# Kernel tuning notes

Measured on AMD Instinct MI355X. Metric: run time of the kernel, lower is better.

Reference implementation:

```python
import jax, jax.numpy as jnp
import numpy as np
from functools import partial

IMAGE_SIZE = 256
ORIG_SIZE = 1024
NEAR, FAR = 0.1, 100.0
CHUNK = 100  # faces processed per scan step to bound memory


def setup_inputs():
    key = jax.random.key(0)
    kv, kf = jax.random.split(key)
    B, V, F = 4, 5000, 10000
    verts = jax.random.normal(kv, (B, V, 3), jnp.float32) * 0.4
    verts = verts.at[..., 2].add(2.5)  # object in front of camera (+z)
    faces = jax.random.randint(kf, (B, F, 3), 0, V)
    fx = fy = float(ORIG_SIZE)
    cx = cy = ORIG_SIZE / 2.0
    K = jnp.broadcast_to(jnp.array([[fx, 0., cx], [0., fy, cy], [0., 0., 1.]], jnp.float32), (B, 3, 3))
    R = jnp.broadcast_to(jnp.eye(3, dtype=jnp.float32), (B, 3, 3))
    t = jnp.zeros((B, 1, 3), jnp.float32)
    dist_coeffs = jnp.zeros((B, 5), jnp.float32)
    return {"vertices": verts, "faces": faces, "K": K, "R": R, "t": t, "dist_coeffs": dist_coeffs}


def projection(vertices, K, R, t, dist_coeffs, orig_size, eps=1e-9):
    # vertices: [B,V,3]; matmul(vertices, R^T) + t, OpenCV distortion, intrinsics, NDC
    v = jnp.einsum('bvj,bij->bvi', vertices, R) + t
    x, y, z = v[..., 0], v[..., 1], v[..., 2]
    x_ = x / (z + eps)
    y_ = y / (z + eps)
    k1, k2, p1, p2, k3 = [dist_coeffs[:, i:i + 1] for i in range(5)]
    r2 = x_ * x_ + y_ * y_
    rad = 1. + k1 * r2 + k2 * r2 * r2 + k3 * r2 * r2 * r2
    x__ = x_ * rad + 2. * p1 * x_ * y_ + p2 * (r2 + 2. * x_ * x_)
    y__ = y_ * rad + p1 * (r2 + 2. * y_ * y_) + 2. * p2 * x_ * y_
    vv = jnp.stack([x__, y__, jnp.ones_like(z)], axis=-1)
    vv = jnp.einsum('bvj,bij->bvi', vv, K)
    u, vc = vv[..., 0], vv[..., 1]
    vc = orig_size - vc  # image y points down
    u = 2. * (u - orig_size / 2.) / orig_size
    vc = 2. * (vc - orig_size / 2.) / orig_size
    return jnp.stack([u, vc, z], axis=-1)  # [B,V,3] in NDC xy, camera z


def vertices_to_faces(vertices, faces):
    # vertices [B,V,3], faces [B,F,3] -> [B,F,3,3]
    return jnp.take_along_axis(vertices[:, :, None, :], faces[:, :, :, None], axis=1)


def rasterize_depth(face_verts, image_size, near, far):
    # face_verts: [B,F,3,3]; z-buffer min of barycentric-interpolated 1/z depth
    B, F = face_verts.shape[:2]
    pad = (-F) % CHUNK
    fv = jnp.pad(face_verts, ((0, 0), (0, pad), (0, 0), (0, 0)))  # padded faces are degenerate
    n_chunks = (F + pad) // CHUNK
    fv = fv.reshape(B, n_chunks, CHUNK, 3, 3).transpose(1, 0, 2, 3, 4)  # [n,B,C,3,3]
    ps = (2. * jnp.arange(image_size, dtype=jnp.float32) + 1. - image_size) / image_size
    xp = ps[None, None, None, :]  # [1,1,1,W]
    yp = ps[None, None, :, None]  # [1,1,H,1]
    eps = 1e-8

    def step(zbuf, chunk):  # chunk [B,C,3,3]
        x = chunk[..., 0]
        y = chunk[..., 1]
        z = chunk[..., 2]
        x0, x1, x2 = (x[..., i, None, None] for i in range(3))
        y0, y1, y2 = (y[..., i, None, None] for i in range(3))
        z0, z1, z2 = (z[..., i, None, None] for i in range(3))
        denom = (y1 - y2) * (x0 - x2) + (x2 - x1) * (y0 - y2)
        ok = jnp.abs(denom) > eps
        safe_d = jnp.where(ok, denom, 1.)
        w0 = ((y1 - y2) * (xp - x2) + (x2 - x1) * (yp - y2)) / safe_d  # [B,C,H,W]
        w1 = ((y2 - y0) * (xp - x2) + (x0 - x2) * (yp - y2)) / safe_d
        w2 = 1. - w0 - w1
        inside = (w0 >= 0.) & (w1 >= 0.) & (w2 >= 0.) & ok
        zs0 = jnp.where(z0 > eps, z0, 1.)
        zs1 = jnp.where(z1 > eps, z1, 1.)
        zs2 = jnp.where(z2 > eps, z2, 1.)
        zinv = w0 / zs0 + w1 / zs1 + w2 / zs2
        zp = 1. / jnp.where(zinv > eps, zinv, 1.)
        valid = inside & (zp > near) & (zp < far) & (z0 > eps) & (z1 > eps) & (z2 > eps)
        zp = jnp.where(valid, zp, far)
        zbuf = jnp.minimum(zbuf, jnp.min(zp, axis=1))  # min over faces in chunk
        return zbuf, None

    zbuf0 = jnp.full((B, image_size, image_size), far, dtype=face_verts.dtype)
    zbuf, _ = jax.lax.scan(step, zbuf0, fv)
    return zbuf[:, ::-1, :]  # flip vertically to image convention


def reference(vertices, faces, K, R, t, dist_coeffs):
    # fill_back: append faces with reversed winding
    faces_fb = jnp.concatenate([faces, faces[:, :, ::-1]], axis=1)
    v_ndc = projection(vertices, K, R, t, dist_coeffs, float(ORIG_SIZE))
    fverts = vertices_to_faces(v_ndc, faces_fb)  # [B,2F,3,3]
    return rasterize_depth(fverts, IMAGE_SIZE, NEAR, FAR)  # [B,H,W] depth map
```

## Files before the change

### kernel.cpp

```cpp
#include <hip/hip_runtime.h>

#define IMG 256
#define TW 32
#define TH 32
#define TILES 64
#define SUBSPLIT 16
#define RSUB 8
#define BIGF 1e30f

typedef float v4f __attribute__((ext_vector_type(4)));

__device__ __forceinline__ float ndc(int i) { return (2.0f*i + 1.0f - IMG) * (1.0f/IMG); }

__device__ __forceinline__ void rank_to_tile(int rank, int& tx, int& ty) {
    int k, base;
    if (rank < 4)       { k = 0; base = 0;  }
    else if (rank < 16) { k = 1; base = 4;  }
    else if (rank < 36) { k = 2; base = 16; }
    else                { k = 3; base = 36; }
    int j = rank - base;
    int s = 2*k + 2;
    int seg = j / (s - 1);
    int off = j - seg * (s - 1);
    int lo = 3 - k, hi = 4 + k;
    if      (seg == 0) { tx = lo + off; ty = lo; }
    else if (seg == 1) { tx = hi;       ty = lo + off; }
    else if (seg == 2) { tx = hi - off; ty = hi; }
    else               { tx = lo;       ty = hi - off; }
}

__device__ __forceinline__ bool tile_test(v4f gx, v4f gy, v4f a,
                                          float txlo, float txhi, float tylo, float tyhi) {
    float m0 = fmaxf(gx.x*txlo, gx.x*txhi) + fmaxf(gy.x*tylo, gy.x*tyhi) + a.x;
    float m1 = fmaxf(gx.y*txlo, gx.y*txhi) + fmaxf(gy.y*tylo, gy.y*tyhi) + a.y;
    float m2 = fmaxf(gx.z*txlo, gx.z*txhi) + fmaxf(gy.z*tylo, gy.z*tyhi) + a.z;
    return fminf(fminf(m0, m1), m2) >= -1e-5f;
}

__device__ __forceinline__ float plane_min(float gw, float hw, float aw,
                                           float xlo, float xhi, float ylo, float yhi) {
    return fminf(gw*xlo, gw*xhi) + fminf(hw*ylo, hw*yhi) + aw;
}

__device__ __forceinline__ float wave_max_dpp(float v) {
    int x;
    x = __builtin_amdgcn_update_dpp(0, __float_as_int(v), 0x111, 0xF, 0xF, true);
    v = fmaxf(v, __int_as_float(x));
    x = __builtin_amdgcn_update_dpp(0, __float_as_int(v), 0x112, 0xF, 0xF, true);
    v = fmaxf(v, __int_as_float(x));
    x = __builtin_amdgcn_update_dpp(0, __float_as_int(v), 0x114, 0xF, 0xF, true);
    v = fmaxf(v, __int_as_float(x));
    x = __builtin_amdgcn_update_dpp(0, __float_as_int(v), 0x118, 0xF, 0xF, true);
    v = fmaxf(v, __int_as_float(x));
    x = __builtin_amdgcn_update_dpp(0, __float_as_int(v), 0x142, 0xF, 0xF, true);
    v = fmaxf(v, __int_as_float(x));
    x = __builtin_amdgcn_update_dpp(0, __float_as_int(v), 0x143, 0xF, 0xF, true);
    v = fmaxf(v, __int_as_float(x));
    return __int_as_float(__builtin_amdgcn_readlane(__float_as_int(v), 63));
}

__device__ __forceinline__ unsigned long long cover_mask_px(int i0, int i1, int j0, int j1,
                                                            v4f gx, v4f gy, v4f aa) {
    if (i0 > 255 || i1 < 0 || j0 > 255 || j1 < 0) return 0ull;
    int tx0 = max(i0, 0) >> 5, tx1 = min(i1, 255) >> 5;
    int ty0 = max(j0, 0) >> 5, ty1 = min(j1, 255) >> 5;
    unsigned long long m = 0ull;
    for (int ty = ty0; ty <= ty1; ++ty) {
        float tylo = ndc(ty*TH), tyhi = ndc(ty*TH + TH - 1);
        for (int tx = tx0; tx <= tx1; ++tx) {
            if (tile_test(gx, gy, aa, ndc(tx*TW), ndc(tx*TW + TW - 1), tylo, tyhi))
                m |= 1ull << (ty*8 + tx);
        }
    }
    return m;
}

__global__ void k_prep(const float* __restrict__ verts, const int* __restrict__ faces,
                       const float* __restrict__ Km, const float* __restrict__ Rm,
                       const float* __restrict__ tm, const float* __restrict__ dm,
                       v4f* __restrict__ fd, v4f* __restrict__ bb,
                       unsigned int* __restrict__ ids,
                       unsigned int* __restrict__ outz, unsigned int* __restrict__ gcnt,
                       int B, int V, int F, int nz, int faceBlocks, int doBins) {
    if ((int)blockIdx.x >= faceBlocks) {
        int idx = (blockIdx.x - faceBlocks) * 256 + threadIdx.x;
        int stride = (gridDim.x - faceBlocks) * 256;
        for (int j = idx; j < nz; j += stride) outz[j] = 0x42C80000u;
        return;
    }
    __shared__ int lcnt[1024];
    __shared__ unsigned int lbase[1024];
    __shared__ int lofs[1024];
    int nbins = TILES * B;
    int tid = threadIdx.x;
    if (doBins) {
        for (int k = tid; k < nbins; k += 256) { lcnt[k] = 0; lofs[k] = 0; }
        __syncthreads();
    }
    int i = blockIdx.x * 256 + tid;
    bool alive = i < B * F;
    unsigned long long tmask = 0ull;
    int b = 0, j0c = 0, j1c = 0;
    if (alive) {
        b = i / F;
        const float* vb = verts + (size_t)b * V * 3;
        const float* R = Rm + b * 9;
        const float* K = Km + b * 9;
        const float* t = tm + b * 3;
        const float* d = dm + b * 5;
        float X[3], Y[3], Z[3];
        #pragma unroll
        for (int c = 0; c < 3; ++c) {
            int vi = faces[3*i + c];
            float px = vb[3*vi], py = vb[3*vi+1], pz = vb[3*vi+2];
            float x = R[0]*px + R[1]*py + R[2]*pz + t[0];
            float y = R[3]*px + R[4]*py + R[5]*pz + t[1];
            float z = R[6]*px + R[7]*py + R[8]*pz + t[2];
            float iz = 1.0f / (z + 1e-9f);
            float x_ = x * iz, y_ = y * iz;
            float k1 = d[0], k2 = d[1], p1 = d[2], p2 = d[3], k3 = d[4];
            float r2 = x_*x_ + y_*y_;
            float rad = 1.0f + k1*r2 + k2*r2*r2 + k3*r2*r2*r2;
            float xd = x_*rad + 2.0f*p1*x_*y_ + p2*(r2 + 2.0f*x_*x_);
            float yd = y_*rad + p1*(r2 + 2.0f*y_*y_) + 2.0f*p2*x_*y_;
            float u  = K[0]*xd + K[1]*yd + K[2];
            float vc = K[3]*xd + K[4]*yd + K[5];
            vc = 1024.0f - vc;
            X[c] = (u  - 512.0f) * (1.0f/512.0f);
            Y[c] = (vc - 512.0f) * (1.0f/512.0f);
            Z[c] = z;
        }
        float x0=X[0], y0=Y[0], z0=Z[0], x1=X[1], y1=Y[1], z1=Z[1], x2=X[2], y2=Y[2], z2=Z[2];
        float denom = (y1-y2)*(x0-x2) + (x2-x1)*(y0-y2);
        bool ok = (fabsf(denom) > 1e-8f) && (z0 > 1e-8f) && (z1 > 1e-8f) && (z2 > 1e-8f);
        if (!ok) {
            bb[i] = (v4f){3e38f, -3e38f, 3e38f, -3e38f};
        } else {
            float s = (denom > 0.0f) ? 1.0f : -1.0f;
            float absd = fabsf(denom);
            float P0x = s*(y1-y2), P0y = s*(x2-x1);
            float P1x = s*(y2-y0), P1y = s*(x0-x2);
            float P2x = -(P0x + P1x), P2y = -(P0y + P1y);
            float A0 = -(P0x*x2 + P0y*y2);
            float A1 = -(P1x*x2 + P1y*y2);
            float A2 = absd - A0 - A1;
            float ia  = 1.0f / absd;
            float rz0 = ia / z0, rz1 = ia / z1, rz2 = ia / z2;
            float zix = P0x*rz0 + P1x*rz1 + P2x*rz2;
            float ziy = P0y*rz0 + P1y*rz1 + P2y*rz2;
            float zic = A0*rz0 + A1*rz1 + A2*rz2;
            v4f ga = (v4f){P0x, P1x, P2x, -zix};
            v4f gb = (v4f){P0y, P1y, P2y, -ziy};
            v4f gc = (v4f){A0,  A1,  A2,  10.0f - zic};
            fd[(size_t)i*3 + 0] = ga;
            fd[(size_t)i*3 + 1] = gb;
            fd[(size_t)i*3 + 2] = gc;
            float xmn = fminf(x0, fminf(x1, x2)) - 1e-4f;
            float xmx = fmaxf(x0, fmaxf(x1, x2)) + 1e-4f;
            float ymn = fminf(y0, fminf(y1, y2)) - 1e-4f;
            float ymx = fmaxf(y0, fmaxf(y1, y2)) + 1e-4f;
            bb[i] = (v4f){xmn, xmx, ymn, ymx};
            if (doBins) {
                int i0 = (int)floorf(xmn*128.0f + 127.5f);
                int i1 = (int)ceilf (xmx*128.0f + 127.5f);
                int j0 = (int)floorf(ymn*128.0f + 127.5f);
                int j1 = (int)ceilf (ymx*128.0f + 127.5f);
                tmask = cover_mask_px(i0, i1, j0, j1, ga, gb, gc);
                j0c = max(j0, 0); j1c = min(j1, 255);
            }
        }
    }
    if (doBins) {
        unsigned long long mk = tmask;
        while (mk) {
            int t = __builtin_ctzll(mk); mk &= mk - 1ull;
            atomicAdd(&lcnt[t*B + b], 1);
        }
        __syncthreads();
        for (int k = tid; k < nbins; k += 256)
            if (lcnt[k]) lbase[k] = atomicAdd(&gcnt[k], (unsigned int)lcnt[k]);
        __syncthreads();
        mk = tmask;
        while (mk) {
            int t = __builtin_ctzll(mk); mk &= mk - 1ull;
            int ty = t >> 3;
            int bin = t*B + b;
            unsigned int blo = (unsigned int)max((j0c >> 3) - ty*4, 0);
            unsigned int bhi = (unsigned int)min((j1c >> 3) - ty*4, 3);
            unsigned int pack = (unsigned int)i | (blo << 28) | (bhi << 30);
            int sl = atomicAdd(&lofs[bin], 1);
            ids[(size_t)bin*F + lbase[bin] + sl] = pack;
        }
    }
}

__global__ __launch_bounds__(256) void k_raster(const v4f* __restrict__ fd,
                                                const unsigned int* __restrict__ ids,
                                                const unsigned int* __restrict__ gcnt,
                                                unsigned int* __restrict__ outz,
                                                int B, int F) {
    __shared__ v4f sA[257], sB[257], sC[257];
    int tid = threadIdx.x, lane = tid & 63, wave = tid >> 6;
    int wbase = wave << 6;
    int tbIdx = blockIdx.x >> 3;
    int sub = blockIdx.x & (RSUB-1);
    int rank = tbIdx / B;
    int b = tbIdx - rank * B;
    int tx, ty;
    rank_to_tile(rank, tx, ty);
    int bin = (ty*8 + tx)*B + b;
    unsigned int len = gcnt[bin];
    size_t base = (size_t)bin * F;
    unsigned int p0 = (unsigned int)(((unsigned long long)sub     * len) / RSUB);
    unsigned int p1 = (unsigned int)(((unsigned long long)(sub+1) * len) / RSUB);

    int rowbase = ty*TH + wave*8;
    int row = rowbase + (lane >> 3);
    int col = tx*TW + (lane & 7) * 4;
    float yp = ndc(row);
    float xp[4];
    #pragma unroll
    for (int jj = 0; jj < 4; ++jj) xp[jj] = ndc(col + jj);
    float txlo = ndc(tx*TW), txhi = ndc(tx*TW + TW - 1);
    float bylo = ndc(rowbase), byhi = ndc(rowbase + 7);
    float m[4] = {BIGF, BIGF, BIGF, BIGF};

    int orow = IMG - 1 - row;
    size_t zo = (size_t)b * (IMG*IMG) + (size_t)orow * IMG + col;

    float hs = 0.0f;
    #pragma unroll
    for (int jj = 0; jj < 4; ++jj) {
        float d = __uint_as_float(outz[zo + jj]);
        hs = fmaxf(hs, 10.0f - 1.0f/d);
    }
    float h = fminf(9.99f, wave_max_dpp(hs) + 1e-4f);

    if (p1 > p0) {
        unsigned int pc = ids[base + min(p0 + lane, p1 - 1)];
        bool vc = (p0 + lane) < p1;
        unsigned int pn = ids[base + min(p0 + 64 + lane, p1 - 1)];
        bool vn = (p0 + 64 + lane) < p1;

        for (unsigned int p = p0; p < p1; p += 64) {
            unsigned int p2w = ids[base + min(p + 128 + lane, p1 - 1)];
            bool v2 = (p + 128 + lane) < p1;

            unsigned int blo = (pc >> 28) & 3u, bhi = pc >> 30;
            unsigned int idc = pc & 0x0FFFFFFFu;
            bool pass = vc & ((int)blo <= wave) & ((int)bhi >= wave);
            bool full = false;
            v4f ra = (v4f){0,0,0,0}, rb = (v4f){0,0,0,0}, rc = (v4f){0,0,0,0};
            if (pass) {
                ra = fd[(size_t)idc*3]; rb = fd[(size_t)idc*3+1]; rc = fd[(size_t)idc*3+2];
                float p0l=ra.x*txlo, p0h=ra.x*txhi, q0l=rb.x*bylo, q0h=rb.x*byhi;
                float p1l=ra.y*txlo, p1h=ra.y*txhi, q1l=rb.y*bylo, q1h=rb.y*byhi;
                float p2l=ra.z*txlo, p2h=ra.z*txhi, q2l=rb.z*bylo, q2h=rb.z*byhi;
                float c0x = fmaxf(p0l,p0h) + fmaxf(q0l,q0h) + rc.x;
                float c1x = fmaxf(p1l,p1h) + fmaxf(q1l,q1h) + rc.y;
                float c2x = fmaxf(p2l,p2h) + fmaxf(q2l,q2h) + rc.z;
                float c0n = fminf(p0l,p0h) + fminf(q0l,q0h) + rc.x;
                float c1n = fminf(p1l,p1h) + fminf(q1l,q1h) + rc.y;
                float c2n = fminf(p2l,p2h) + fminf(q2l,q2h) + rc.z;
                float zmn = fminf(ra.w*txlo, ra.w*txhi) + fminf(rb.w*bylo, rb.w*byhi) + rc.w;
                pass = (fminf(fminf(c0x, c1x), c2x) >= -1e-5f) & (zmn < h);
                full = (fminf(fminf(c0n, c1n), c2n) >= 1e-5f);
            }
            unsigned long long mp = __ballot(pass && !full);
            unsigned long long mf = __ballot(pass && full);
            int cp = __popcll(mp);
            int cf = __popcll(mf);
            if (pass && !full) {
                int sl = wbase + __popcll(mp & ((1ull << lane) - 1ull));
                sA[sl] = ra; sB[sl] = rb; sC[sl] = rc;
            }
            unsigned long long w = mf;
            while (w) {
                int l = __builtin_amdgcn_readfirstlane(__ffsll((unsigned long long)w) - 1);
                w &= w - 1ull;
                float gxw = __int_as_float(__builtin_amdgcn_readlane(__float_as_int(ra.w), l));
                float gyw = __int_as_float(__builtin_amdgcn_readlane(__float_as_int(rb.w), l));
                float aaw = __int_as_float(__builtin_amdgcn_readlane(__float_as_int(rc.w), l));
                float e3 = fmaf(gyw, yp, aaw);
                #pragma unroll
                for (int jj = 0; jj < 4; ++jj)
                    m[jj] = fminf(m[jj], fmaf(gxw, xp[jj], e3));
            }
            if (cp > 0) {
                v4f gx = sA[wbase], gy = sB[wbase], aa = sC[wbase];
                for (int i = 0; i < cp; ++i) {
                    v4f nx = sA[wbase+i+1], ny = sB[wbase+i+1], nzv = sC[wbase+i+1];
                    float e0 = fmaf(gy.x, yp, aa.x);
                    float e1 = fmaf(gy.y, yp, aa.y);
                    float e2 = fmaf(gy.z, yp, aa.z);
                    float e3 = fmaf(gy.w, yp, aa.w);
                    #pragma unroll
                    for (int jj = 0; jj < 4; ++jj) {
                        float n0 = fmaf(gx.x, xp[jj], e0);
                        float n1 = fmaf(gx.y, xp[jj], e1);
                        float n2 = fmaf(gx.z, xp[jj], e2);
                        float n3 = fmaf(gx.w, xp[jj], e3);
                        float q = fminf(fminf(n0, n1), n2);
                        m[jj] = fminf(m[jj], (q >= 0.0f) ? n3 : BIGF);
                    }
                    gx = nx; gy = ny; aa = nzv;
                }
            }
            if (cp + cf > 0)
                h = fminf(9.99f, wave_max_dpp(fmaxf(fmaxf(m[0], m[1]), fmaxf(m[2], m[3]))));
            pc = pn; vc = vn;
            pn = p2w; vn = v2;
        }
    }
    #pragma unroll
    for (int jj = 0; jj < 4; ++jj) {
        if (m[jj] < 9.99f) {
            float depth = 1.0f / (10.0f - m[jj]);
            unsigned int mv = __float_as_uint(depth);
            unsigned int cv = outz[zo + jj];
            if (mv < cv) atomicMin(&outz[zo + jj], mv);
        }
    }
}

__global__ __launch_bounds__(256) void k_raster_scan(const v4f* __restrict__ fd,
                                                     const v4f* __restrict__ bb,
                                                     unsigned int* __restrict__ outz,
                                                     int B, int F) {
    __shared__ v4f sA[257], sB[257], sC[257];
    int tid = threadIdx.x, lane = tid & 63, wave = tid >> 6;
    int wbase = wave << 6;
    int j = blockIdx.x >> 4;
    int s = blockIdx.x & (SUBSPLIT-1);
    int nTB = TILES * B;
    int f_begin = (s * F) / SUBSPLIT, f_end = ((s + 1) * F) / SUBSPLIT;

    #pragma unroll 1
    for (int phase = 0; phase < 2; ++phase) {
        int tb = (phase == 0) ? j : (nTB - 1 - j);
        int rank = tb / B;
        int b = tb - rank * B;
        int tx, ty;
        rank_to_tile(rank, tx, ty);
        int rowbase = ty*TH + wave*8;
        int row = rowbase + (lane >> 3);
        int col = tx*TW + (lane & 7) * 4;
        float yp = ndc(row);
        float xp[4];
        #pragma unroll
        for (int jj = 0; jj < 4; ++jj) xp[jj] = ndc(col + jj);
        float txlo = ndc(tx*TW), txhi = ndc(tx*TW + TW - 1);
        float bylo = ndc(rowbase), byhi = ndc(rowbase + 7);
        float m[4] = {BIGF, BIGF, BIGF, BIGF};
        float h = 9.99f;

        const v4f* bbp = bb + (size_t)b * F;
        const v4f* fdp = fd + (size_t)b * F * 3;

        v4f box = bbp[min(f_begin + lane, f_end - 1)];
        bool valid = (f_begin + lane) < f_end;

        for (int g0 = f_begin; g0 < f_end; g0 += 64) {
            int fn = g0 + 64 + lane;
            v4f nbox = bbp[min(fn, f_end - 1)];
            bool nvalid = fn < f_end;

            bool pass = valid &
                        (box.x <= txhi) & (box.y >= txlo) &
                        (box.z <= byhi) & (box.w >= bylo);
            v4f ra, rb, rc;
            if (pass) {
                int f = g0 + lane;
                ra = fdp[3*f]; rb = fdp[3*f+1]; rc = fdp[3*f+2];
                pass = tile_test(ra, rb, rc, txlo, txhi, bylo, byhi)
                    && (plane_min(ra.w, rb.w, rc.w, txlo, txhi, bylo, byhi) < h);
            }
            unsigned long long mk = __ballot(pass);
            int total = __popcll(mk);
            if (pass) {
                int slot = wbase + __popcll(mk & ((1ull << lane) - 1ull));
                sA[slot] = ra;
                sB[slot] = rb;
                sC[slot] = rc;
            }
            if (total > 0) {
                v4f gx = sA[wbase], gy = sB[wbase], aa = sC[wbase];
                for (int i = 0; i < total; ++i) {
                    v4f nx = sA[wbase+i+1], ny = sB[wbase+i+1], nzv = sC[wbase+i+1];
                    float e0 = fmaf(gy.x, yp, aa.x);
                    float e1 = fmaf(gy.y, yp, aa.y);
                    float e2 = fmaf(gy.z, yp, aa.z);
                    float e3 = fmaf(gy.w, yp, aa.w);
                    #pragma unroll
                    for (int jj = 0; jj < 4; ++jj) {
                        float n0 = fmaf(gx.x, xp[jj], e0);
                        float n1 = fmaf(gx.y, xp[jj], e1);
                        float n2 = fmaf(gx.z, xp[jj], e2);
                        float n3 = fmaf(gx.w, xp[jj], e3);
                        float q = fminf(fminf(n0, n1), n2);
                        m[jj] = fminf(m[jj], (q >= 0.0f) ? n3 : BIGF);
                    }
                    gx = nx; gy = ny; aa = nzv;
                }
                h = fminf(9.99f, wave_max_dpp(fmaxf(fmaxf(m[0], m[1]), fmaxf(m[2], m[3]))));
            }
            box = nbox; valid = nvalid;
        }
        int orow = IMG - 1 - row;
        size_t zo = (size_t)b * (IMG*IMG) + (size_t)orow * IMG + col;
        #pragma unroll
        for (int jj = 0; jj < 4; ++jj) {
            if (m[jj] < 9.99f) {
                float depth = 1.0f / (10.0f - m[jj]);
                unsigned int mv = __float_as_uint(depth);
                unsigned int cv = outz[zo + jj];
                if (mv < cv) atomicMin(&outz[zo + jj], mv);
            }
        }
    }
}

extern "C" void kernel_launch(void* const* d_in, const int* in_sizes, int n_in,
                              void* d_out, int out_size, void* d_ws, size_t ws_size,
                              hipStream_t stream) {
    const float* verts = (const float*)d_in[0];
    const int*   faces = (const int*)d_in[1];
    const float* Km    = (const float*)d_in[2];
    const float* Rm    = (const float*)d_in[3];
    const float* tm    = (const float*)d_in[4];
    const float* dm    = (const float*)d_in[5];
    float* out = (float*)d_out;

    int B = in_sizes[2] / 9;
    int V = in_sizes[0] / (3 * B);
    int F = in_sizes[1] / (3 * B);
    int nz = B * IMG * IMG;
    int nbins = TILES * B;

    char* ws = (char*)d_ws;
    size_t al = 255;
    size_t o_fd  = 0;
    size_t o_bb  = (o_fd + (size_t)B*F*48 + al) & ~al;
    size_t o_cnt = (o_bb + (size_t)B*F*16 + al) & ~al;
    size_t o_ids = (o_cnt + (size_t)nbins*4 + al) & ~al;
    size_t need_bins = o_ids + (size_t)nbins * F * 4;
    size_t need_scan = o_ids;

    v4f* fd  = (v4f*)(ws + o_fd);
    v4f* bbp = (v4f*)(ws + o_bb);
    unsigned int* gcnt = (unsigned int*)(ws + o_cnt);
    unsigned int* ids  = (unsigned int*)(ws + o_ids);

    const int thr = 256;
    int faceBlocks = (B*F + thr - 1) / thr;

    if (ws_size >= need_bins && nbins <= 1024 && (size_t)B*F < (1u<<28)) {
        hipMemsetAsync(gcnt, 0, (size_t)nbins*4, stream);
        k_prep<<<faceBlocks + 128, thr, 0, stream>>>(verts, faces, Km, Rm, tm, dm,
                                                     fd, bbp, ids, (unsigned int*)out, gcnt,
                                                     B, V, F, nz, faceBlocks, 1);
        int rasterBlocks = nbins * RSUB;
        k_raster<<<rasterBlocks, thr, 0, stream>>>(fd, ids, gcnt,
                                                   (unsigned int*)out, B, F);
    } else if (ws_size >= need_scan) {
        k_prep<<<faceBlocks + 128, thr, 0, stream>>>(verts, faces, Km, Rm, tm, dm,
                                                     fd, bbp, ids, (unsigned int*)out, gcnt,
                                                     B, V, F, nz, faceBlocks, 0);
        int rasterBlocks = (TILES * B / 2) * SUBSPLIT;
        k_raster_scan<<<rasterBlocks, thr, 0, stream>>>(fd, bbp, (unsigned int*)out, B, F);
    }
}
```

Baseline: 116.4 us.

## Balance raster work via global prefix scan of bin counts across fixed blocks

```diff
diff --git a/kernel.cpp b/kernel.cpp
--- a/kernel.cpp
+++ b/kernel.cpp
@@ -5,7 +5,7 @@
 #define TH 32
 #define TILES 64
 #define SUBSPLIT 16
-#define RSUB 8
+#define NRB 2048
 #define BIGF 1e30f
 
 typedef float v4f __attribute__((ext_vector_type(4)));
@@ -75,7 +75,8 @@
     return m;
 }
 
-__global__ void k_prep(const float* __restrict__ verts, const int* __restrict__ faces,
+__global__ __launch_bounds__(64) void k_prep(const float* __restrict__ verts,
+                       const int* __restrict__ faces,
                        const float* __restrict__ Km, const float* __restrict__ Rm,
                        const float* __restrict__ tm, const float* __restrict__ dm,
                        v4f* __restrict__ fd, v4f* __restrict__ bb,
@@ -83,8 +84,8 @@
                        unsigned int* __restrict__ outz, unsigned int* __restrict__ gcnt,
                        int B, int V, int F, int nz, int faceBlocks, int doBins) {
     if ((int)blockIdx.x >= faceBlocks) {
-        int idx = (blockIdx.x - faceBlocks) * 256 + threadIdx.x;
-        int stride = (gridDim.x - faceBlocks) * 256;
+        int idx = (blockIdx.x - faceBlocks) * 64 + threadIdx.x;
+        int stride = (gridDim.x - faceBlocks) * 64;
         for (int j = idx; j < nz; j += stride) outz[j] = 0x42C80000u;
         return;
     }
@@ -94,10 +95,10 @@
     int nbins = TILES * B;
     int tid = threadIdx.x;
     if (doBins) {
-        for (int k = tid; k < nbins; k += 256) { lcnt[k] = 0; lofs[k] = 0; }
+        for (int k = tid; k < nbins; k += 64) { lcnt[k] = 0; lofs[k] = 0; }
         __syncthreads();
     }
-    int i = blockIdx.x * 256 + tid;
+    int i = blockIdx.x * 64 + tid;
     bool alive = i < B * F;
     unsigned long long tmask = 0ull;
     int b = 0, j0c = 0, j1c = 0;
@@ -177,7 +178,7 @@
             atomicAdd(&lcnt[t*B + b], 1);
         }
         __syncthreads();
-        for (int k = tid; k < nbins; k += 256)
+        for (int k = tid; k < nbins; k += 64)
             if (lcnt[k]) lbase[k] = atomicAdd(&gcnt[k], (unsigned int)lcnt[k]);
         __syncthreads();
         mk = tmask;
@@ -194,49 +195,88 @@
     }
 }
 
+__global__ __launch_bounds__(256) void k_scan(const unsigned int* __restrict__ gcnt,
+                                              unsigned int* __restrict__ goff, int nbins) {
+    __shared__ unsigned int ps[256];
+    int tid = threadIdx.x;
+    unsigned int loc[4], s = 0;
+    #pragma unroll
+    for (int k = 0; k < 4; ++k) {
+        int idx = tid*4 + k;
+        unsigned int c = (idx < nbins) ? gcnt[idx] : 0u;
+        loc[k] = c; s += c;
+    }
+    ps[tid] = s; __syncthreads();
+    #pragma unroll
+    for (int d = 1; d < 256; d <<= 1) {
+        unsigned int t = (tid >= d) ? ps[tid - d] : 0u;
+        __syncthreads();
+        ps[tid] += t;
+        __syncthreads();
+    }
+    unsigned int run = ps[tid] - s;
+    #pragma unroll
+    for (int k = 0; k < 4; ++k) {
+        int idx = tid*4 + k;
+        if (idx < nbins) {
+            goff[idx] = run; run += loc[k];
+            if (idx == nbins - 1) goff[nbins] = run;
+        }
+    }
+}
+
 __global__ __launch_bounds__(256) void k_raster(const v4f* __restrict__ fd,
                                                 const unsigned int* __restrict__ ids,
-                                                const unsigned int* __restrict__ gcnt,
+                                                const unsigned int* __restrict__ goff,
                                                 unsigned int* __restrict__ outz,
-                                                int B, int F) {
+                                                int B, int F, int nbins) {
     __shared__ v4f sA[257], sB[257], sC[257];
     int tid = threadIdx.x, lane = tid & 63, wave = tid >> 6;
     int wbase = wave << 6;
-    int tbIdx = blockIdx.x >> 3;
-    int sub = blockIdx.x & (RSUB-1);
-    int rank = tbIdx / B;
-    int b = tbIdx - rank * B;
-    int tx, ty;
-    rank_to_tile(rank, tx, ty);
-    int bin = (ty*8 + tx)*B + b;
-    unsigned int len = gcnt[bin];
-    size_t base = (size_t)bin * F;
-    unsigned int p0 = (unsigned int)(((unsigned long long)sub     * len) / RSUB);
-    unsigned int p1 = (unsigned int)(((unsigned long long)(sub+1) * len) / RSUB);
-
-    int rowbase = ty*TH + wave*8;
-    int row = rowbase + (lane >> 3);
-    int col = tx*TW + (lane & 7) * 4;
-    float yp = ndc(row);
-    float xp[4];
-    #pragma unroll
-    for (int jj = 0; jj < 4; ++jj) xp[jj] = ndc(col + jj);
-    float txlo = ndc(tx*TW), txhi = ndc(tx*TW + TW - 1);
-    float bylo = ndc(rowbase), byhi = ndc(rowbase + 7);
-    float m[4] = {BIGF, BIGF, BIGF, BIGF};
-
-    int orow = IMG - 1 - row;
-    size_t zo = (size_t)b * (IMG*IMG) + (size_t)orow * IMG + col;
-
-    float hs = 0.0f;
-    #pragma unroll
-    for (int jj = 0; jj < 4; ++jj) {
-        float d = __uint_as_float(outz[zo + jj]);
-        hs = fmaxf(hs, 10.0f - 1.0f/d);
-    }
-    float h = fminf(9.99f, wave_max_dpp(hs) + 1e-4f);
-
-    if (p1 > p0) {
+    unsigned int T = goff[nbins];
+    if (T == 0) return;
+    unsigned int g0 = (unsigned int)(((unsigned long long)blockIdx.x     * T) / NRB);
+    unsigned int g1 = (unsigned int)(((unsigned long long)(blockIdx.x+1) * T) / NRB);
+    if (g1 <= g0) return;
+
+    int lo = 0, hi = nbins;
+    while (hi - lo > 1) { int mid = (lo + hi) >> 1; if (goff[mid] <= g0) lo = mid; else hi = mid; }
+    int bin = lo;
+    unsigned int g = g0;
+
+    while (g < g1) {
+        unsigned int boff = goff[bin], bend = goff[bin+1];
+        if (bend <= boff || bend <= g) { ++bin; continue; }
+        unsigned int p0 = g - boff;
+        unsigned int p1 = min(bend, g1) - boff;
+
+        int t = bin / B;
+        int b = bin - t * B;
+        int ty = t >> 3, tx = t & 7;
+        size_t base = (size_t)bin * F;
+
+        int rowbase = ty*TH + wave*8;
+        int row = rowbase + (lane >> 3);
+        int col = tx*TW + (lane & 7) * 4;
+        float yp = ndc(row);
+        float xp[4];
+        #pragma unroll
+        for (int jj = 0; jj < 4; ++jj) xp[jj] = ndc(col + jj);
+        float txlo = ndc(tx*TW), txhi = ndc(tx*TW + TW - 1);
+        float bylo = ndc(rowbase), byhi = ndc(rowbase + 7);
+        float m[4] = {BIGF, BIGF, BIGF, BIGF};
+
+        int orow = IMG - 1 - row;
+        size_t zo = (size_t)b * (IMG*IMG) + (size_t)orow * IMG + col;
+
+        float hs = 0.0f;
+        #pragma unroll
+        for (int jj = 0; jj < 4; ++jj) {
+            float d = __uint_as_float(outz[zo + jj]);
+            hs = fmaxf(hs, 10.0f - 1.0f/d);
+        }
+        float h = fminf(9.99f, wave_max_dpp(hs) + 1e-4f);
+
         unsigned int pc = ids[base + min(p0 + lane, p1 - 1)];
         bool vc = (p0 + lane) < p1;
         unsigned int pn = ids[base + min(p0 + 64 + lane, p1 - 1)];
@@ -307,19 +347,21 @@
                 }
             }
             if (cp + cf > 0)
-                h = fminf(9.99f, wave_max_dpp(fmaxf(fmaxf(m[0], m[1]), fmaxf(m[2], m[3]))));
+                h = fminf(h, wave_max_dpp(fmaxf(fmaxf(m[0], m[1]), fmaxf(m[2], m[3]))));
             pc = pn; vc = vn;
             pn = p2w; vn = v2;
         }
-    }
-    #pragma unroll
-    for (int jj = 0; jj < 4; ++jj) {
-        if (m[jj] < 9.99f) {
-            float depth = 1.0f / (10.0f - m[jj]);
-            unsigned int mv = __float_as_uint(depth);
-            unsigned int cv = outz[zo + jj];
-            if (mv < cv) atomicMin(&outz[zo + jj], mv);
-        }
+        #pragma unroll
+        for (int jj = 0; jj < 4; ++jj) {
+            if (m[jj] < 9.99f) {
+                float depth = 1.0f / (10.0f - m[jj]);
+                unsigned int mv = __float_as_uint(depth);
+                unsigned int cv = outz[zo + jj];
+                if (mv < cv) atomicMin(&outz[zo + jj], mv);
+            }
+        }
+        g = min(bend, g1);
+        ++bin;
     }
 }
 
@@ -442,31 +484,31 @@
     size_t o_fd  = 0;
     size_t o_bb  = (o_fd + (size_t)B*F*48 + al) & ~al;
     size_t o_cnt = (o_bb + (size_t)B*F*16 + al) & ~al;
-    size_t o_ids = (o_cnt + (size_t)nbins*4 + al) & ~al;
+    size_t o_off = (o_cnt + (size_t)nbins*4 + al) & ~al;
+    size_t o_ids = (o_off + (size_t)(nbins+1)*4 + al) & ~al;
     size_t need_bins = o_ids + (size_t)nbins * F * 4;
-    size_t need_scan = o_ids;
+    size_t need_scan = o_cnt;
 
     v4f* fd  = (v4f*)(ws + o_fd);
     v4f* bbp = (v4f*)(ws + o_bb);
     unsigned int* gcnt = (unsigned int*)(ws + o_cnt);
+    unsigned int* goff = (unsigned int*)(ws + o_off);
     unsigned int* ids  = (unsigned int*)(ws + o_ids);
 
-    const int thr = 256;
-    int faceBlocks = (B*F + thr - 1) / thr;
+    int faceBlocks = (B*F + 63) / 64;
 
     if (ws_size >= need_bins && nbins <= 1024 && (size_t)B*F < (1u<<28)) {
         hipMemsetAsync(gcnt, 0, (size_t)nbins*4, stream);
-        k_prep<<<faceBlocks + 128, thr, 0, stream>>>(verts, faces, Km, Rm, tm, dm,
-                                                     fd, bbp, ids, (unsigned int*)out, gcnt,
-                                                     B, V, F, nz, faceBlocks, 1);
-        int rasterBlocks = nbins * RSUB;
-        k_raster<<<rasterBlocks, thr, 0, stream>>>(fd, ids, gcnt,
-                                                   (unsigned int*)out, B, F);
+        k_prep<<<faceBlocks + 256, 64, 0, stream>>>(verts, faces, Km, Rm, tm, dm,
+                                                    fd, bbp, ids, (unsigned int*)out, gcnt,
+                                                    B, V, F, nz, faceBlocks, 1);
+        k_scan<<<1, 256, 0, stream>>>(gcnt, goff, nbins);
+        k_raster<<<NRB, 256, 0, stream>>>(fd, ids, goff, (unsigned int*)out, B, F, nbins);
     } else if (ws_size >= need_scan) {
-        k_prep<<<faceBlocks + 128, thr, 0, stream>>>(verts, faces, Km, Rm, tm, dm,
-                                                     fd, bbp, ids, (unsigned int*)out, gcnt,
-                                                     B, V, F, nz, faceBlocks, 0);
+        k_prep<<<faceBlocks + 256, 64, 0, stream>>>(verts, faces, Km, Rm, tm, dm,
+                                                    fd, bbp, ids, (unsigned int*)out, gcnt,
+                                                    B, V, F, nz, faceBlocks, 0);
         int rasterBlocks = (TILES * B / 2) * SUBSPLIT;
-        k_raster_scan<<<rasterBlocks, thr, 0, stream>>>(fd, bbp, (unsigned int*)out, B, F);
-    }
-}
+        k_raster_scan<<<rasterBlocks, 256, 0, stream>>>(fd, bbp, (unsigned int*)out, B, F);
+    }
+}
```

After: 149.8 us. 28.7% more time.
